# Performance work log

Measured on AMD Instinct MI355X. Metric: run time of the kernel, lower is better.

## Reference

```python
import jax, jax.numpy as jnp
import numpy as np
from functools import partial

B, T, IN, H, NC, L = 2048, 512, 64, 64, 4, 2


def _lstm_layer(x, w_ih, w_hh, b_ih, b_hh):
    """Single PyTorch-convention LSTM layer. x: [B,T,Din]; gates ordered i,f,g,o.
    Returns full hidden sequence [B,T,H]."""
    Bx = x.shape[0]
    Hh = w_hh.shape[1]
    # precompute input contribution for all timesteps: [T,B,4H]
    xg = jnp.einsum('bti,gi->tbg', x, w_ih) + (b_ih + b_hh)

    def step(carry, xg_t):
        h, c = carry
        gates = xg_t + h @ w_hh.T  # [B,4H]
        i, f, g, o = jnp.split(gates, 4, axis=-1)
        i = jax.nn.sigmoid(i)
        f = jax.nn.sigmoid(f)
        g = jnp.tanh(g)
        o = jax.nn.sigmoid(o)
        c = f * c + i * g
        h = o * jnp.tanh(c)
        return (h, c), h

    h0 = jnp.zeros((Bx, Hh), dtype=x.dtype)
    c0 = jnp.zeros((Bx, Hh), dtype=x.dtype)
    (_, _), hs = jax.lax.scan(step, (h0, c0), xg)  # hs: [T,B,H]
    return jnp.swapaxes(hs, 0, 1)  # [B,T,H]


def setup_inputs() -> dict:
    key = jax.random.key(0)
    ks = jax.random.split(key, 16)
    s_in = 1.0 / np.sqrt(H)
    inp = {"x": jax.random.normal(ks[0], (B, T, IN), dtype=jnp.float32)}
    dims = [IN, H]
    for l in range(L):
        inp[f"w_ih{l}"] = jax.random.uniform(ks[1 + 4 * l], (4 * H, dims[l]), jnp.float32, -s_in, s_in)
        inp[f"w_hh{l}"] = jax.random.uniform(ks[2 + 4 * l], (4 * H, H), jnp.float32, -s_in, s_in)
        inp[f"b_ih{l}"] = jax.random.uniform(ks[3 + 4 * l], (4 * H,), jnp.float32, -s_in, s_in)
        inp[f"b_hh{l}"] = jax.random.uniform(ks[4 + 4 * l], (4 * H,), jnp.float32, -s_in, s_in)
    inp["fc_w"] = jax.random.uniform(ks[9], (NC, H), jnp.float32, -s_in, s_in)
    inp["fc_b"] = jax.random.uniform(ks[10], (NC,), jnp.float32, -s_in, s_in)
    return inp


def reference(x, w_ih0, w_hh0, b_ih0, b_hh0, w_ih1, w_hh1, b_ih1, b_hh1, fc_w, fc_b):
    # layer 0
    h1 = _lstm_layer(x, w_ih0, w_hh0, b_ih0, b_hh0)   # [B,T,H]
    # inter-layer dropout: identity at inference
    h2 = _lstm_layer(h1, w_ih1, w_hh1, b_ih1, b_hh1)  # [B,T,H]
    last = h2[:, -1, :]                                # [B,H]; dropout = identity (eval)
    return last @ fc_w.T + fc_b                        # [B,NC]
```

## Files before the change

kernel.cpp:

```cpp
#include <hip/hip_runtime.h>
#include <stdint.h>


#define T_SEQ 512
#define NB    4
#define PSTR  136
#define PANEL (16 * PSTR)

typedef __attribute__((ext_vector_type(8))) short  short8;
typedef __attribute__((ext_vector_type(4))) float  float4v;

__device__ __forceinline__ unsigned short f2bf(float f) {
    unsigned int u = __builtin_bit_cast(unsigned int, f);
    return (unsigned short)((u + 0x7FFFu + ((u >> 16) & 1u)) >> 16);
}
__device__ __forceinline__ unsigned short f2bf_rhu(float f) {
    unsigned int u = __builtin_bit_cast(unsigned int, f);
    return (unsigned short)((u + 0x8000u) >> 16);
}
__device__ __forceinline__ float bf2f(unsigned short h) {
    unsigned int u = ((unsigned int)h) << 16;
    return __builtin_bit_cast(float, u);
}
__device__ __forceinline__ float sigm(float x) {
    return __builtin_amdgcn_rcpf(1.0f + __builtin_amdgcn_exp2f(-1.44269504088896f * x));
}
__device__ __forceinline__ float tanh_f(float x) {
    float e = __builtin_amdgcn_exp2f(-2.88539008177793f * x);
    return __builtin_fmaf(2.0f, __builtin_amdgcn_rcpf(1.0f + e), -1.0f);
}

__global__ __launch_bounds__(512, 4) void lstm2_kernel(
    const float* __restrict__ x,
    const float* __restrict__ wih0, const float* __restrict__ whh0,
    const float* __restrict__ bih0, const float* __restrict__ bhh0,
    const float* __restrict__ wih1, const float* __restrict__ whh1,
    const float* __restrict__ bih1, const float* __restrict__ bhh1,
    const float* __restrict__ fcw,  const float* __restrict__ fcb,
    float* __restrict__ out)
{
    __shared__ __align__(16) unsigned short panel0[2][PANEL];
    __shared__ __align__(16) unsigned short panel1[2][PANEL];
    __shared__ float h2buf[NB * 64];
    __shared__ float fcw_s[256];
    __shared__ float fcb_s[4];

    const int tid  = threadIdx.x;
    const int lane = tid & 63;
    const int wave = tid >> 6;
    const int mrow = lane & 15;
    const int kg   = lane >> 4;
    const int lset = wave >> 2;
    const int ws   = wave & 3;
    const int b0   = blockIdx.x * NB;

    for (int i = tid; i < 256; i += 512) fcw_s[i] = fcw[i];
    if (tid < 4) fcb_s[tid] = fcb[tid];
    for (int i = tid; i < 2 * PANEL; i += 512) {
        panel0[0][i] = 0; panel1[0][i] = 0;
    }

    const float* wih  = lset ? wih1 : wih0;
    const float* whh  = lset ? whh1 : whh0;
    const float* bihp = lset ? bih1 : bih0;
    const float* bhhp = lset ? bhh1 : bhh0;

    float biasg[4];
    #pragma unroll
    for (int g = 0; g < 4; ++g) {
        const int idx = g * 64 + ws * 16 + mrow;
        biasg[g] = bihp[idx] + bhhp[idx];
    }

    short8 whiF[4][4];
    #pragma unroll
    for (int g = 0; g < 4; ++g) {
        const int n = (g * 4 + ws) * 16 + mrow;
        #pragma unroll
        for (int kt = 0; kt < 4; ++kt) {
            const int k0 = kt * 32 + kg * 8;
            const float* src = (k0 < 64) ? (wih + n * 64 + k0)
                                         : (whh + n * 64 + (k0 - 64));
            union { short8 s; unsigned short u[8]; } hi8;
            #pragma unroll
            for (int j = 0; j < 8; ++j) hi8.u[j] = f2bf(src[j]);
            whiF[g][kt] = hi8.s;
        }
    }

    __syncthreads();
    if (tid < 256) {
        const int bx = tid >> 6, kx = tid & 63;
        float xv = x[((size_t)(b0 + bx) * T_SEQ + 0) * 64 + kx];
        unsigned short h = f2bf_rhu(xv);
        panel0[0][(4 * bx) * PSTR + kx]     = h;
        panel0[0][(4 * bx + 1) * PSTR + kx] = f2bf_rhu(xv - bf2f(h));
    }
    __syncthreads();

    const int fragoff = mrow * PSTR + kg * 8;
    const unsigned short* rdA = &panel0[0][0] + (lset ? 64 : 0) + fragoff;
    const unsigned short* rdB = (lset ? &panel1[0][0] : &panel0[0][0]) + fragoff;
    unsigned short* hP = lset ? &panel1[0][0] : &panel0[0][0];
    const int hcol  = ws * 16 + mrow;
    const int hoff0 = (4 * kg) * PSTR + 64 + hcol;
    const int hoff1 = hoff0 + PSTR;
    const int bw    = wave & 3;
    const int xr0   = (4 * bw) * PSTR + lane;
    const float* xp = x + ((size_t)(b0 + bw) * T_SEQ + 1) * 64 + lane;
    float c = 0.f;
    const float4v z4 = {0.f, 0.f, 0.f, 0.f};

    for (int s = 0; s <= T_SEQ; ++s) {
        const int p    = s & 1;
        const int poff = p * PANEL;
        const int qoff = poff ^ PANEL;

        const bool do_stage = (lset == 1) && (s + 1 < T_SEQ);
        float xv = 0.f;
        if (do_stage) xv = *xp;

        short8 af[4];
        {
            const unsigned short* bA = rdA + poff;
            const unsigned short* bB = rdB + poff;
            af[0] = *(const short8*)(bA);
            af[1] = *(const short8*)(bA + 32);
            af[2] = *(const short8*)(bB + 64);
            af[3] = *(const short8*)(bB + 96);
        }
        float4v acc[4];
        #pragma unroll
        for (int g = 0; g < 4; ++g)
            acc[g] = __builtin_amdgcn_mfma_f32_16x16x32_bf16(af[0], whiF[g][0], z4, 0, 0, 0);
        #pragma unroll
        for (int kt = 1; kt < 4; ++kt) {
            #pragma unroll
            for (int g = 0; g < 4; ++g)
                acc[g] = __builtin_amdgcn_mfma_f32_16x16x32_bf16(af[kt], whiF[g][kt], acc[g], 0, 0, 0);
        }

        const bool active = lset ? (s > 0) : (s < T_SEQ);
        if (active) {
            float g0 = acc[0][0] + acc[0][1] + biasg[0];
            float g1 = acc[1][0] + acc[1][1] + biasg[1];
            float g2 = acc[2][0] + acc[2][1] + biasg[2];
            float g3 = acc[3][0] + acc[3][1] + biasg[3];
            float ig = sigm(g0), fg = sigm(g1);
            float gt = tanh_f(g2), og = sigm(g3);
            c = fg * c + ig * gt;
            float hv = og * tanh_f(c);
            unsigned short hhi = f2bf_rhu(hv);
            unsigned short hlo = f2bf_rhu(hv - bf2f(hhi));
            unsigned short* w = hP + qoff;
            w[hoff0] = hhi;
            w[hoff1] = hlo;
            if (lset && s == T_SEQ) h2buf[(kg << 6) + hcol] = hv;
        }
        if (do_stage) {
            unsigned short xh = f2bf_rhu(xv);
            unsigned short xl = f2bf_rhu(xv - bf2f(xh));
            unsigned short* w0 = &panel0[0][0] + qoff + xr0;
            w0[0]    = xh;
            w0[PSTR] = xl;
            xp += 64;
        }
        __syncthreads();
    }

    if (tid < 16) {
        const int bb = tid >> 2, nc = tid & 3;
        float s = fcb_s[nc];
        #pragma unroll 8
        for (int h = 0; h < 64; ++h) s += h2buf[bb * 64 + h] * fcw_s[nc * 64 + h];
        out[(size_t)(b0 + bb) * 4 + nc] = s;
    }
}

extern "C" void kernel_launch(void* const* d_in, const int* in_sizes, int n_in,
                              void* d_out, int out_size, void* d_ws, size_t ws_size,
                              hipStream_t stream) {
    const float* x    = (const float*)d_in[0];
    const float* wih0 = (const float*)d_in[1];
    const float* whh0 = (const float*)d_in[2];
    const float* bih0 = (const float*)d_in[3];
    const float* bhh0 = (const float*)d_in[4];
    const float* wih1 = (const float*)d_in[5];
    const float* whh1 = (const float*)d_in[6];
    const float* bih1 = (const float*)d_in[7];
    const float* bhh1 = (const float*)d_in[8];
    const float* fcw  = (const float*)d_in[9];
    const float* fcb  = (const float*)d_in[10];
    float* out = (float*)d_out;
    (void)d_ws; (void)ws_size; (void)in_sizes; (void)n_in; (void)out_size;

    lstm2_kernel<<<dim3(2048 / NB), dim3(512), 0, stream>>>(
        x, wih0, whh0, bih0, bhh0, wih1, whh1, bih1, bhh1, fcw, fcb, out);
}
```

Before: 667.2 us.

## Switch recurrent MFMA from split-bf16 to fp16 and pack 8 sequences per block

Replaces the hi/lo bf16 split representation of activations with a single fp16 value, freeing the MFMA rows that held the low parts. Those rows now carry a second batch element, so each block handles 8 sequences instead of 4 and each lane keeps two cell states. This halves the number of blocks and the recurrent MFMA work per sequence, at the cost of lower precision for h and x (fp16 without error compensation) and a lower occupancy hint in launch bounds. h2buf is still sized NB*64, which now matches 8 sequences.

```diff
diff --git a/kernel.cpp b/kernel.cpp
--- a/kernel.cpp
+++ b/kernel.cpp
@@ -3,25 +3,13 @@
 
 
 #define T_SEQ 512
-#define NB    4
+#define NB    8
 #define PSTR  136
 #define PANEL (16 * PSTR)
 
-typedef __attribute__((ext_vector_type(8))) short  short8;
-typedef __attribute__((ext_vector_type(4))) float  float4v;
-
-__device__ __forceinline__ unsigned short f2bf(float f) {
-    unsigned int u = __builtin_bit_cast(unsigned int, f);
-    return (unsigned short)((u + 0x7FFFu + ((u >> 16) & 1u)) >> 16);
-}
-__device__ __forceinline__ unsigned short f2bf_rhu(float f) {
-    unsigned int u = __builtin_bit_cast(unsigned int, f);
-    return (unsigned short)((u + 0x8000u) >> 16);
-}
-__device__ __forceinline__ float bf2f(unsigned short h) {
-    unsigned int u = ((unsigned int)h) << 16;
-    return __builtin_bit_cast(float, u);
-}
+typedef __attribute__((ext_vector_type(8))) _Float16 half8;
+typedef __attribute__((ext_vector_type(4))) float    float4v;
+
 __device__ __forceinline__ float sigm(float x) {
     return __builtin_amdgcn_rcpf(1.0f + __builtin_amdgcn_exp2f(-1.44269504088896f * x));
 }
@@ -30,7 +18,7 @@
     return __builtin_fmaf(2.0f, __builtin_amdgcn_rcpf(1.0f + e), -1.0f);
 }
 
-__global__ __launch_bounds__(512, 4) void lstm2_kernel(
+__global__ __launch_bounds__(512, 2) void lstm2_kernel(
     const float* __restrict__ x,
     const float* __restrict__ wih0, const float* __restrict__ whh0,
     const float* __restrict__ bih0, const float* __restrict__ bhh0,
@@ -72,7 +60,7 @@
         biasg[g] = bihp[idx] + bhhp[idx];
     }
 
-    short8 whiF[4][4];
+    half8 whiF[4][4];
     #pragma unroll
     for (int g = 0; g < 4; ++g) {
         const int n = (g * 4 + ws) * 16 + mrow;
@@ -81,20 +69,22 @@
             const int k0 = kt * 32 + kg * 8;
             const float* src = (k0 < 64) ? (wih + n * 64 + k0)
                                          : (whh + n * 64 + (k0 - 64));
-            union { short8 s; unsigned short u[8]; } hi8;
+            half8 hv8;
             #pragma unroll
-            for (int j = 0; j < 8; ++j) hi8.u[j] = f2bf(src[j]);
-            whiF[g][kt] = hi8.s;
+            for (int j = 0; j < 8; ++j) hv8[j] = (_Float16)src[j];
+            whiF[g][kt] = hv8;
         }
     }
 
     __syncthreads();
     if (tid < 256) {
-        const int bx = tid >> 6, kx = tid & 63;
-        float xv = x[((size_t)(b0 + bx) * T_SEQ + 0) * 64 + kx];
-        unsigned short h = f2bf_rhu(xv);
-        panel0[0][(4 * bx) * PSTR + kx]     = h;
-        panel0[0][(4 * bx + 1) * PSTR + kx] = f2bf_rhu(xv - bf2f(h));
+        const int bx = tid >> 5, c0 = (tid & 31) * 2;
+        const int row = 4 * (bx >> 1) + (bx & 1);
+        const float* xs = x + ((size_t)(b0 + bx) * T_SEQ + 0) * 64 + c0;
+        union { _Float16 h[2]; unsigned int u; } p2;
+        p2.h[0] = (_Float16)xs[0];
+        p2.h[1] = (_Float16)xs[1];
+        *(unsigned int*)&panel0[0][row * PSTR + c0] = p2.u;
     }
     __syncthreads();
 
@@ -103,12 +93,14 @@
     const unsigned short* rdB = (lset ? &panel1[0][0] : &panel0[0][0]) + fragoff;
     unsigned short* hP = lset ? &panel1[0][0] : &panel0[0][0];
     const int hcol  = ws * 16 + mrow;
-    const int hoff0 = (4 * kg) * PSTR + 64 + hcol;
-    const int hoff1 = hoff0 + PSTR;
-    const int bw    = wave & 3;
-    const int xr0   = (4 * bw) * PSTR + lane;
-    const float* xp = x + ((size_t)(b0 + bw) * T_SEQ + 1) * 64 + lane;
-    float c = 0.f;
+    const int hoffA = (4 * kg) * PSTR + 64 + hcol;
+    const int hoffB = hoffA + PSTR;
+    const int st   = ((wave & 3) << 6) + lane;
+    const int sbx  = st >> 5;
+    const int sc0  = (st & 31) * 2;
+    const int sxof = (4 * (sbx >> 1) + (sbx & 1)) * PSTR + sc0;
+    const float* xp = x + ((size_t)(b0 + sbx) * T_SEQ + 1) * 64 + sc0;
+    float cA = 0.f, cB = 0.f;
     const float4v z4 = {0.f, 0.f, 0.f, 0.f};
 
     for (int s = 0; s <= T_SEQ; ++s) {
@@ -117,58 +109,68 @@
         const int qoff = poff ^ PANEL;
 
         const bool do_stage = (lset == 1) && (s + 1 < T_SEQ);
-        float xv = 0.f;
-        if (do_stage) xv = *xp;
-
-        short8 af[4];
+        float xv0 = 0.f, xv1 = 0.f;
+        if (do_stage) { xv0 = xp[0]; xv1 = xp[1]; }
+
+        half8 af[4];
         {
             const unsigned short* bA = rdA + poff;
             const unsigned short* bB = rdB + poff;
-            af[0] = *(const short8*)(bA);
-            af[1] = *(const short8*)(bA + 32);
-            af[2] = *(const short8*)(bB + 64);
-            af[3] = *(const short8*)(bB + 96);
+            af[0] = *(const half8*)(bA);
+            af[1] = *(const half8*)(bA + 32);
+            af[2] = *(const half8*)(bB + 64);
+            af[3] = *(const half8*)(bB + 96);
         }
         float4v acc[4];
         #pragma unroll
         for (int g = 0; g < 4; ++g)
-            acc[g] = __builtin_amdgcn_mfma_f32_16x16x32_bf16(af[0], whiF[g][0], z4, 0, 0, 0);
+            acc[g] = __builtin_amdgcn_mfma_f32_16x16x32_f16(af[0], whiF[g][0], z4, 0, 0, 0);
         #pragma unroll
         for (int kt = 1; kt < 4; ++kt) {
             #pragma unroll
             for (int g = 0; g < 4; ++g)
-                acc[g] = __builtin_amdgcn_mfma_f32_16x16x32_bf16(af[kt], whiF[g][kt], acc[g], 0, 0, 0);
+                acc[g] = __builtin_amdgcn_mfma_f32_16x16x32_f16(af[kt], whiF[g][kt], acc[g], 0, 0, 0);
         }
 
         const bool active = lset ? (s > 0) : (s < T_SEQ);
         if (active) {
-            float g0 = acc[0][0] + acc[0][1] + biasg[0];
-            float g1 = acc[1][0] + acc[1][1] + biasg[1];
-            float g2 = acc[2][0] + acc[2][1] + biasg[2];
-            float g3 = acc[3][0] + acc[3][1] + biasg[3];
-            float ig = sigm(g0), fg = sigm(g1);
-            float gt = tanh_f(g2), og = sigm(g3);
-            c = fg * c + ig * gt;
-            float hv = og * tanh_f(c);
-            unsigned short hhi = f2bf_rhu(hv);
-            unsigned short hlo = f2bf_rhu(hv - bf2f(hhi));
             unsigned short* w = hP + qoff;
-            w[hoff0] = hhi;
-            w[hoff1] = hlo;
-            if (lset && s == T_SEQ) h2buf[(kg << 6) + hcol] = hv;
+            {
+                float g0 = acc[0][0] + biasg[0];
+                float g1 = acc[1][0] + biasg[1];
+                float g2 = acc[2][0] + biasg[2];
+                float g3 = acc[3][0] + biasg[3];
+                float ig = sigm(g0), fg = sigm(g1);
+                float gt = tanh_f(g2), og = sigm(g3);
+                cA = fg * cA + ig * gt;
+                float hv = og * tanh_f(cA);
+                w[hoffA] = __builtin_bit_cast(unsigned short, (_Float16)hv);
+                if (lset && s == T_SEQ) h2buf[(2 * kg) * 64 + hcol] = hv;
+            }
+            {
+                float g0 = acc[0][1] + biasg[0];
+                float g1 = acc[1][1] + biasg[1];
+                float g2 = acc[2][1] + biasg[2];
+                float g3 = acc[3][1] + biasg[3];
+                float ig = sigm(g0), fg = sigm(g1);
+                float gt = tanh_f(g2), og = sigm(g3);
+                cB = fg * cB + ig * gt;
+                float hv = og * tanh_f(cB);
+                w[hoffB] = __builtin_bit_cast(unsigned short, (_Float16)hv);
+                if (lset && s == T_SEQ) h2buf[(2 * kg + 1) * 64 + hcol] = hv;
+            }
         }
         if (do_stage) {
-            unsigned short xh = f2bf_rhu(xv);
-            unsigned short xl = f2bf_rhu(xv - bf2f(xh));
-            unsigned short* w0 = &panel0[0][0] + qoff + xr0;
-            w0[0]    = xh;
-            w0[PSTR] = xl;
+            union { _Float16 h[2]; unsigned int u; } p2;
+            p2.h[0] = (_Float16)xv0;
+            p2.h[1] = (_Float16)xv1;
+            *(unsigned int*)(&panel0[0][0] + qoff + sxof) = p2.u;
             xp += 64;
         }
         __syncthreads();
     }
 
-    if (tid < 16) {
+    if (tid < 32) {
         const int bb = tid >> 2, nc = tid & 3;
         float s = fcb_s[nc];
         #pragma unroll 8
```

Result: slower. 759.3 us (+13.8%).
